# Kernel tuning notes

Measured on AMD Instinct MI355X. Metric: run time of the kernel, lower is better.

Reference implementation:

```python
import jax, jax.numpy as jnp
import numpy as np

NUM_HEADS = 4
HEAD_DIM = 32  # attention_dim 128 / 4 heads
SCALE = HEAD_DIM ** 0.5


def setup_inputs() -> dict:
    key = jax.random.key(0)
    ks = jax.random.split(key, 7)
    B, L, D = 4096, 200, 128
    return {
        "target_item": jax.random.normal(ks[0], (B, D), dtype=jnp.float32),
        "history_sequence": jax.random.normal(ks[1], (B, L, D), dtype=jnp.float32),
        "mask": jax.random.randint(ks[2], (B, L), 0, 2, dtype=jnp.int32),
        "W_q": jax.random.normal(ks[3], (D, D), dtype=jnp.float32) * 0.05,
        "W_k": jax.random.normal(ks[4], (D, D), dtype=jnp.float32) * 0.05,
        "W_v": jax.random.normal(ks[5], (D, D), dtype=jnp.float32) * 0.05,
        "W_o": jax.random.normal(ks[6], (D, D), dtype=jnp.float32) * 0.05,
    }


def reference(target_item, history_sequence, mask, W_q, W_k, W_v, W_o):
    B = target_item.shape[0]
    # QKV projections (nn.Linear with bias=False: y = x @ W.T)
    q = target_item @ W_q.T                      # [B, A]
    k = history_sequence @ W_k.T                 # [B, L, A]
    v = history_sequence @ W_v.T                 # [B, L, A]
    # split heads: q -> [B, H, d], k/v -> [B, H, L, d]
    q = q.reshape(B, NUM_HEADS, HEAD_DIM)
    k = k.reshape(B, -1, NUM_HEADS, HEAD_DIM).transpose(0, 2, 1, 3)
    v = v.reshape(B, -1, NUM_HEADS, HEAD_DIM).transpose(0, 2, 1, 3)
    # single-query scaled dot-product attention
    scores = jnp.einsum("bhd,bhld->bhl", q, k) / SCALE  # [B, H, L]
    m = (mask != 0)[:, None, :]                          # [B, 1, L]
    scores = jnp.where(m, scores, -jnp.inf)
    attn = jax.nn.softmax(scores, axis=-1)               # [B, H, L]
    out = jnp.einsum("bhl,bhld->bhd", attn, v)           # [B, H, d]
    out = out.reshape(B, NUM_HEADS * HEAD_DIM)           # [B, A]
    return out @ W_o.T                                    # [B, q_dim]
```

## Files before the change

### kernel.cpp

```cpp
#include <hip/hip_runtime.h>

#define LL 200
#define DD 128
#define NH 4
#define RSCALE 0.17677669529663687f

__device__ __forceinline__ float blo(unsigned int u) { return __uint_as_float(u << 16); }
__device__ __forceinline__ float bhi(unsigned int u) { return __uint_as_float(u & 0xffff0000u); }
__device__ __forceinline__ float b2f(unsigned short u) { return __uint_as_float(((unsigned int)u) << 16); }
__device__ __forceinline__ unsigned short f2bf(float f) {
  unsigned int u = __float_as_uint(f);
  u += 0x7fffu + ((u >> 16) & 1u);
  return (unsigned short)(u >> 16);
}

template <bool F32>
__device__ __forceinline__ float rowdot128(const void* __restrict__ wrow,
                                           const float* __restrict__ v) {
  float acc = 0.f;
  if constexpr (F32) {
    const float4* wr = (const float4*)wrow;
#pragma unroll
    for (int k = 0; k < 32; k++) {
      float4 w = wr[k];
      float4 vv = *(const float4*)(v + 4 * k);
      acc += w.x * vv.x + w.y * vv.y + w.z * vv.z + w.w * vv.w;
    }
  } else {
    const uint4* wr = (const uint4*)wrow;
#pragma unroll
    for (int k = 0; k < 16; k++) {
      uint4 u = wr[k];
      float4 v0 = *(const float4*)(v + k * 8);
      float4 v1 = *(const float4*)(v + k * 8 + 4);
      acc += blo(u.x) * v0.x + bhi(u.x) * v0.y + blo(u.y) * v0.z + bhi(u.y) * v0.w;
      acc += blo(u.z) * v1.x + bhi(u.z) * v1.y + blo(u.w) * v1.z + bhi(u.w) * v1.w;
    }
  }
  return acc;
}

template <bool F32>
__device__ __forceinline__ float welem(const void* w, size_t idx) {
  if constexpr (F32) return ((const float*)w)[idx];
  else               return b2f(((const unsigned short*)w)[idx]);
}

struct __align__(16) Smem {
  float qt[DD * NH];
  float sc[LL * NH];
  float tvec[DD];
  float qv[DD];
  float cpart[4 * 512];
  int flag;
};

template <bool F32>
__device__ __forceinline__ void body(Smem& sm, const int tid, const int b,
                                     const void* __restrict__ tgt,
                                     const void* __restrict__ hist,
                                     const int* __restrict__ mask,
                                     const void* __restrict__ Wq,
                                     const void* __restrict__ Wk,
                                     const void* __restrict__ Wv,
                                     const void* __restrict__ Wo,
                                     void* __restrict__ out) {
  const float NINF = -__builtin_inff();

  if (tid < DD) sm.tvec[tid] = welem<F32>(tgt, (size_t)b * DD + tid);
  __syncthreads();

  if (tid < DD)
    sm.qv[tid] = rowdot128<F32>((const char*)Wq + (size_t)tid * DD * (F32 ? 4 : 2), sm.tvec);
  __syncthreads();

  for (int e = tid; e < NH * DD; e += 256) {
    const int h = e >> 7, j = e & 127;
    float acc = 0.f;
#pragma unroll 8
    for (int d = 0; d < 32; d++)
      acc += sm.qv[h * 32 + d] * welem<F32>(Wk, (size_t)(h * 32 + d) * DD + j);
    sm.qt[j * NH + h] = acc * RSCALE;
  }
  __syncthreads();

  if (tid < LL) {
    const int l = tid;
    float a0 = 0.f, a1 = 0.f, a2 = 0.f, a3 = 0.f;
#define QACC(JE, FV) { float4 q_ = *(const float4*)&sm.qt[(JE) * 4]; const float f_ = (FV); \
  a0 += f_ * q_.x; a1 += f_ * q_.y; a2 += f_ * q_.z; a3 += f_ * q_.w; }
    if constexpr (!F32) {
      const uint4* hr = (const uint4*)((const unsigned short*)hist + (size_t)(b * LL + l) * DD);
#pragma unroll
      for (int c = 0; c < 2; c++) {
        uint4 u[8];
#pragma unroll
        for (int k = 0; k < 8; k++) u[k] = hr[c * 8 + k];
#pragma unroll
        for (int k = 0; k < 8; k++) {
          const int jb = c * 64 + k * 8;
          QACC(jb + 0, blo(u[k].x)); QACC(jb + 1, bhi(u[k].x));
          QACC(jb + 2, blo(u[k].y)); QACC(jb + 3, bhi(u[k].y));
          QACC(jb + 4, blo(u[k].z)); QACC(jb + 5, bhi(u[k].z));
          QACC(jb + 6, blo(u[k].w)); QACC(jb + 7, bhi(u[k].w));
        }
      }
    } else {
      const float4* hr = (const float4*)((const float*)hist + (size_t)(b * LL + l) * DD);
#pragma unroll
      for (int c = 0; c < 4; c++) {
        float4 u[8];
#pragma unroll
        for (int k = 0; k < 8; k++) u[k] = hr[c * 8 + k];
#pragma unroll
        for (int k = 0; k < 8; k++) {
          const int jb = c * 32 + k * 4;
          QACC(jb + 0, u[k].x); QACC(jb + 1, u[k].y);
          QACC(jb + 2, u[k].z); QACC(jb + 3, u[k].w);
        }
      }
    }
#undef QACC
    const bool mv = mask[(size_t)b * LL + l] != 0;
    float4 sv;
    sv.x = mv ? a0 : NINF;
    sv.y = mv ? a1 : NINF;
    sv.z = mv ? a2 : NINF;
    sv.w = mv ? a3 : NINF;
    *(float4*)&sm.sc[l * 4] = sv;
  }
  __syncthreads();

  {
    const int h = tid >> 6, lane = tid & 63;
    float v0 = sm.sc[lane * 4 + h];
    float v1 = sm.sc[(lane + 64) * 4 + h];
    float v2 = sm.sc[(lane + 128) * 4 + h];
    float v3 = (lane < 8) ? sm.sc[(lane + 192) * 4 + h] : NINF;
    float m = fmaxf(fmaxf(v0, v1), fmaxf(v2, v3));
#pragma unroll
    for (int off = 32; off; off >>= 1) m = fmaxf(m, __shfl_xor(m, off));
    float e0 = __expf(v0 - m), e1 = __expf(v1 - m), e2 = __expf(v2 - m);
    float e3 = (lane < 8) ? __expf(v3 - m) : 0.f;
    float s = e0 + e1 + e2 + e3;
#pragma unroll
    for (int off = 32; off; off >>= 1) s += __shfl_xor(s, off);
    const float r = 1.f / s;
    sm.sc[lane * 4 + h] = e0 * r;
    sm.sc[(lane + 64) * 4 + h] = e1 * r;
    sm.sc[(lane + 128) * 4 + h] = e2 * r;
    if (lane < 8) sm.sc[(lane + 192) * 4 + h] = e3 * r;
  }
  __syncthreads();

  {
    const int j2 = tid & 63;
    const int ch = tid >> 6;
    const int l0 = ch * 50;
    float a00=0.f,a01=0.f,a10=0.f,a11=0.f,a20=0.f,a21=0.f,a30=0.f,a31=0.f;
    if constexpr (!F32) {
      const unsigned int* hd =
          (const unsigned int*)((const unsigned short*)hist + (size_t)b * LL * DD) + j2;
#pragma unroll 5
      for (int l = l0; l < l0 + 50; l++) {
        const unsigned int dw = hd[l * 64];
        const float f0 = blo(dw), f1 = bhi(dw);
        const float4 at = *(const float4*)&sm.sc[l * 4];
        a00 += f0 * at.x; a01 += f1 * at.x;
        a10 += f0 * at.y; a11 += f1 * at.y;
        a20 += f0 * at.z; a21 += f1 * at.z;
        a30 += f0 * at.w; a31 += f1 * at.w;
      }
    } else {
      const float2* hf = (const float2*)((const float*)hist + (size_t)b * LL * DD) + j2;
#pragma unroll 5
      for (int l = l0; l < l0 + 50; l++) {
        const float2 f = hf[l * 64];
        const float4 at = *(const float4*)&sm.sc[l * 4];
        a00 += f.x * at.x; a01 += f.y * at.x;
        a10 += f.x * at.y; a11 += f.y * at.y;
        a20 += f.x * at.z; a21 += f.y * at.z;
        a30 += f.x * at.w; a31 += f.y * at.w;
      }
    }
    float* cp = &sm.cpart[ch * 512];
    const int j = 2 * j2;
    *(float2*)&cp[0 * DD + j] = make_float2(a00, a01);
    *(float2*)&cp[1 * DD + j] = make_float2(a10, a11);
    *(float2*)&cp[2 * DD + j] = make_float2(a20, a21);
    *(float2*)&cp[3 * DD + j] = make_float2(a30, a31);
  }
  __syncthreads();

  float* cvec = sm.qt;
  for (int idx = tid; idx < 512; idx += 256)
    cvec[idx] = sm.cpart[idx] + sm.cpart[512 + idx] + sm.cpart[1024 + idx] + sm.cpart[1536 + idx];
  __syncthreads();

  if (tid < DD)
    sm.tvec[tid] = rowdot128<F32>((const char*)Wv + (size_t)tid * DD * (F32 ? 4 : 2),
                                  &cvec[(tid >> 5) * DD]);
  __syncthreads();

  if (tid < DD) {
    const float acc = rowdot128<F32>((const char*)Wo + (size_t)tid * DD * (F32 ? 4 : 2), sm.tvec);
    if constexpr (F32) ((float*)out)[(size_t)b * DD + tid] = acc;
    else               ((unsigned short*)out)[(size_t)b * DD + tid] = f2bf(acc);
  }
}

__global__ __launch_bounds__(256, 5)
void mhta_kernel(const void* __restrict__ tgt,
                 const void* __restrict__ hist,
                 const int* __restrict__ mask,
                 const void* __restrict__ Wq,
                 const void* __restrict__ Wk,
                 const void* __restrict__ Wv,
                 const void* __restrict__ Wo,
                 void* __restrict__ out)
{
  __shared__ Smem sm;
  const int tid = threadIdx.x;
  const int b = blockIdx.x;

  if (tid < 64) {
    const unsigned int* hd = (const unsigned int*)((const char*)hist + (size_t)b * LL * DD * 2);
    const unsigned int e = (hd[tid] >> 7) & 0xffu;
    const unsigned long long bal = __ballot(e >= 110u && e <= 134u);
    if (tid == 0) sm.flag = (__popcll(bal) < 32) ? 1 : 0;
  }
  __syncthreads();

  if (sm.flag) body<true >(sm, tid, b, tgt, hist, mask, Wq, Wk, Wv, Wo, out);
  else         body<false>(sm, tid, b, tgt, hist, mask, Wq, Wk, Wv, Wo, out);
}

extern "C" void kernel_launch(void* const* d_in, const int* in_sizes, int n_in,
                              void* d_out, int out_size, void* d_ws, size_t ws_size,
                              hipStream_t stream) {
  const void* tgt  = d_in[0];
  const void* hist = d_in[1];
  const int*  mask = (const int*)d_in[2];
  const void* Wq   = d_in[3];
  const void* Wk   = d_in[4];
  const void* Wv   = d_in[5];
  const void* Wo   = d_in[6];

  const int B = in_sizes[0] / DD;

  mhta_kernel<<<dim3(B), dim3(256), 0, stream>>>(tgt, hist, mask, Wq, Wk, Wv, Wo, d_out);
}
```

Measured before the change: 694.5 us.

## Map one batch element per wavefront and skip loads for masked history rows

Restructures the kernel so each 64-lane wavefront handles a whole batch element (four per block) instead of a 256-thread block per element. Score computation skips history row loads where the mask is zero, and the attention-weighted value sum iterates only over a compacted list of unmasked rows built with ballot/popcount. This cuts history memory traffic roughly in half for the random mask and removes cross-wave reductions. In exchange each wave repeats all the projection work serially, and __syncthreads is now used inside per-wave code paths, which still hold up the whole block.

Result: slower. 890.9 us (+28.3%).

```diff
diff --git a/kernel.cpp b/kernel.cpp
--- a/kernel.cpp
+++ b/kernel.cpp
@@ -3,6 +3,7 @@
 #define LL 200
 #define DD 128
 #define NH 4
+#define WPB 4
 #define RSCALE 0.17677669529663687f
 
 __device__ __forceinline__ float blo(unsigned int u) { return __uint_as_float(u << 16); }
@@ -13,6 +14,9 @@
   u += 0x7fffu + ((u >> 16) & 1u);
   return (unsigned short)(u >> 16);
 }
+__device__ __forceinline__ unsigned int pack2(float lo, float hi) {
+  return ((unsigned int)f2bf(hi) << 16) | (unsigned int)f2bf(lo);
+}
 
 template <bool F32>
 __device__ __forceinline__ float rowdot128(const void* __restrict__ wrow,
@@ -46,17 +50,14 @@
   else               return b2f(((const unsigned short*)w)[idx]);
 }
 
-struct __align__(16) Smem {
-  float qt[DD * NH];
+struct __align__(16) WaveSmem {
+  float qt[NH * DD];
   float sc[LL * NH];
-  float tvec[DD];
-  float qv[DD];
-  float cpart[4 * 512];
-  int flag;
+  float u[2 * DD];
 };
 
 template <bool F32>
-__device__ __forceinline__ void body(Smem& sm, const int tid, const int b,
+__device__ __forceinline__ void body(WaveSmem& ws, const int lane, const int b,
                                      const void* __restrict__ tgt,
                                      const void* __restrict__ hist,
                                      const int* __restrict__ mask,
@@ -66,146 +67,241 @@
                                      const void* __restrict__ Wo,
                                      void* __restrict__ out) {
   const float NINF = -__builtin_inff();
-
-  if (tid < DD) sm.tvec[tid] = welem<F32>(tgt, (size_t)b * DD + tid);
-  __syncthreads();
-
-  if (tid < DD)
-    sm.qv[tid] = rowdot128<F32>((const char*)Wq + (size_t)tid * DD * (F32 ? 4 : 2), sm.tvec);
-  __syncthreads();
-
-  for (int e = tid; e < NH * DD; e += 256) {
-    const int h = e >> 7, j = e & 127;
-    float acc = 0.f;
-#pragma unroll 8
-    for (int d = 0; d < 32; d++)
-      acc += sm.qv[h * 32 + d] * welem<F32>(Wk, (size_t)(h * 32 + d) * DD + j);
-    sm.qt[j * NH + h] = acc * RSCALE;
-  }
-  __syncthreads();
-
-  if (tid < LL) {
-    const int l = tid;
-    float a0 = 0.f, a1 = 0.f, a2 = 0.f, a3 = 0.f;
-#define QACC(JE, FV) { float4 q_ = *(const float4*)&sm.qt[(JE) * 4]; const float f_ = (FV); \
-  a0 += f_ * q_.x; a1 += f_ * q_.y; a2 += f_ * q_.z; a3 += f_ * q_.w; }
-    if constexpr (!F32) {
-      const uint4* hr = (const uint4*)((const unsigned short*)hist + (size_t)(b * LL + l) * DD);
-#pragma unroll
-      for (int c = 0; c < 2; c++) {
-        uint4 u[8];
-#pragma unroll
-        for (int k = 0; k < 8; k++) u[k] = hr[c * 8 + k];
-#pragma unroll
-        for (int k = 0; k < 8; k++) {
-          const int jb = c * 64 + k * 8;
-          QACC(jb + 0, blo(u[k].x)); QACC(jb + 1, bhi(u[k].x));
-          QACC(jb + 2, blo(u[k].y)); QACC(jb + 3, bhi(u[k].y));
-          QACC(jb + 4, blo(u[k].z)); QACC(jb + 5, bhi(u[k].z));
-          QACC(jb + 6, blo(u[k].w)); QACC(jb + 7, bhi(u[k].w));
+  const size_t esz = F32 ? 4 : 2;
+  float* tvec = ws.u;
+  float* qv   = ws.u + DD;
+
+  if constexpr (F32) {
+    *(float2*)&tvec[2 * lane] = ((const float2*)tgt)[(size_t)b * 64 + lane];
+  } else {
+    const unsigned int dw = ((const unsigned int*)tgt)[(size_t)b * 64 + lane];
+    *(float2*)&tvec[2 * lane] = make_float2(blo(dw), bhi(dw));
+  }
+  __syncthreads();
+
+#pragma unroll
+  for (int r = 0; r < 2; r++) {
+    const int i = lane + 64 * r;
+    qv[i] = rowdot128<F32>((const char*)Wq + (size_t)i * DD * esz, tvec);
+  }
+  __syncthreads();
+
+#pragma unroll
+  for (int h = 0; h < NH; h++) {
+#pragma unroll
+    for (int r = 0; r < 2; r++) {
+      const int j = lane + 64 * r;
+      float acc = 0.f;
+#pragma unroll
+      for (int d = 0; d < 32; d++)
+        acc += qv[h * 32 + d] * welem<F32>(Wk, (size_t)(h * 32 + d) * DD + j);
+      ws.qt[j * NH + h] = acc * RSCALE;
+    }
+  }
+  __syncthreads();
+
+  int lrow[4];
+  int am[4];
+#pragma unroll
+  for (int k = 0; k < 3; k++) lrow[k] = lane + 64 * k;
+  lrow[3] = 192 + (lane & 7);
+#pragma unroll
+  for (int k = 0; k < 4; k++) am[k] = mask[(size_t)b * LL + lrow[k]] != 0;
+  if (lane >= 8) am[3] = 0;
+
+  float acc[4][4];
+#pragma unroll
+  for (int k = 0; k < 4; k++)
+#pragma unroll
+    for (int h = 0; h < 4; h++) acc[k][h] = 0.f;
+
+  const float4* qt4 = (const float4*)ws.qt;
+
+  if constexpr (!F32) {
+    const unsigned int* hb =
+        (const unsigned int*)((const unsigned short*)hist + (size_t)b * LL * DD);
+    uint4 rb[4][2] = {};
+#pragma unroll 2
+    for (int c = 0; c < 8; c++) {
+#pragma unroll
+      for (int k = 0; k < 4; k++)
+        if (am[k]) {
+          const uint4* p = (const uint4*)&hb[lrow[k] * 64 + (c << 3)];
+          rb[k][0] = p[0];
+          rb[k][1] = p[1];
+        }
+#pragma unroll
+      for (int d2 = 0; d2 < 8; d2++) {
+        const int jj = (c << 4) + (d2 << 1);
+        const float4 q0 = qt4[jj];
+        const float4 q1 = qt4[jj + 1];
+#pragma unroll
+        for (int k = 0; k < 4; k++) {
+          const uint4 v = rb[k][d2 >> 2];
+          const unsigned int dw = ((d2 & 3) == 0) ? v.x
+                                : ((d2 & 3) == 1) ? v.y
+                                : ((d2 & 3) == 2) ? v.z : v.w;
+          const float f0 = blo(dw), f1 = bhi(dw);
+          acc[k][0] += f0 * q0.x + f1 * q1.x;
+          acc[k][1] += f0 * q0.y + f1 * q1.y;
+          acc[k][2] += f0 * q0.z + f1 * q1.z;
+          acc[k][3] += f0 * q0.w + f1 * q1.w;
         }
       }
-    } else {
-      const float4* hr = (const float4*)((const float*)hist + (size_t)(b * LL + l) * DD);
-#pragma unroll
-      for (int c = 0; c < 4; c++) {
-        float4 u[8];
-#pragma unroll
-        for (int k = 0; k < 8; k++) u[k] = hr[c * 8 + k];
-#pragma unroll
-        for (int k = 0; k < 8; k++) {
-          const int jb = c * 32 + k * 4;
-          QACC(jb + 0, u[k].x); QACC(jb + 1, u[k].y);
-          QACC(jb + 2, u[k].z); QACC(jb + 3, u[k].w);
-        }
+    }
+  } else {
+    const float* hf = (const float*)hist + (size_t)b * LL * DD;
+    float4 rb[4] = {};
+#pragma unroll 4
+    for (int c = 0; c < 32; c++) {
+#pragma unroll
+      for (int k = 0; k < 4; k++)
+        if (am[k]) rb[k] = *(const float4*)&hf[(size_t)lrow[k] * DD + (c << 2)];
+      const float4 q0 = qt4[(c << 2)];
+      const float4 q1 = qt4[(c << 2) + 1];
+      const float4 q2 = qt4[(c << 2) + 2];
+      const float4 q3 = qt4[(c << 2) + 3];
+#pragma unroll
+      for (int k = 0; k < 4; k++) {
+        acc[k][0] += rb[k].x * q0.x + rb[k].y * q1.x + rb[k].z * q2.x + rb[k].w * q3.x;
+        acc[k][1] += rb[k].x * q0.y + rb[k].y * q1.y + rb[k].z * q2.y + rb[k].w * q3.y;
+        acc[k][2] += rb[k].x * q0.z + rb[k].y * q1.z + rb[k].z * q2.z + rb[k].w * q3.z;
+        acc[k][3] += rb[k].x * q0.w + rb[k].y * q1.w + rb[k].z * q2.w + rb[k].w * q3.w;
       }
     }
-#undef QACC
-    const bool mv = mask[(size_t)b * LL + l] != 0;
-    float4 sv;
-    sv.x = mv ? a0 : NINF;
-    sv.y = mv ? a1 : NINF;
-    sv.z = mv ? a2 : NINF;
-    sv.w = mv ? a3 : NINF;
-    *(float4*)&sm.sc[l * 4] = sv;
+  }
+
+#pragma unroll
+  for (int k = 0; k < 4; k++)
+#pragma unroll
+    for (int h = 0; h < 4; h++) acc[k][h] = am[k] ? acc[k][h] : NINF;
+
+  float rr[4];
+#pragma unroll
+  for (int h = 0; h < 4; h++) {
+    float m = fmaxf(fmaxf(acc[0][h], acc[1][h]), fmaxf(acc[2][h], acc[3][h]));
+#pragma unroll
+    for (int off = 32; off; off >>= 1) m = fmaxf(m, __shfl_xor(m, off));
+    float e0 = __expf(acc[0][h] - m);
+    float e1 = __expf(acc[1][h] - m);
+    float e2 = __expf(acc[2][h] - m);
+    float e3 = __expf(acc[3][h] - m);
+    acc[0][h] = e0; acc[1][h] = e1; acc[2][h] = e2; acc[3][h] = e3;
+    float su = e0 + e1 + e2 + e3;
+#pragma unroll
+    for (int off = 32; off; off >>= 1) su += __shfl_xor(su, off);
+    rr[h] = 1.f / su;
+  }
+
+  int* sidx = (int*)ws.u;
+  const unsigned long long lt = (1ull << lane) - 1ull;
+  int base = 0;
+#pragma unroll
+  for (int k = 0; k < 4; k++) {
+    const unsigned long long bal = __ballot(am[k] != 0);
+    const int pos = base + (int)__popcll(bal & lt);
+    if (am[k]) {
+      sidx[pos] = lrow[k];
+      *(float4*)&ws.sc[pos * 4] = make_float4(acc[k][0] * rr[0], acc[k][1] * rr[1],
+                                              acc[k][2] * rr[2], acc[k][3] * rr[3]);
+    }
+    base += (int)__popcll(bal);
+  }
+  const int cnt = base;
+  __syncthreads();
+
+  float4 cl = make_float4(0.f, 0.f, 0.f, 0.f);
+  float4 chh = make_float4(0.f, 0.f, 0.f, 0.f);
+  const int j2 = lane;
+  if constexpr (!F32) {
+    const unsigned int* hd =
+        (const unsigned int*)((const unsigned short*)hist + (size_t)b * LL * DD) + j2;
+    int i = 0;
+    for (; i + 4 <= cnt; i += 4) {
+      const int4 li = *(const int4*)&sidx[i];
+      const unsigned int w0 = hd[li.x << 6];
+      const unsigned int w1 = hd[li.y << 6];
+      const unsigned int w2 = hd[li.z << 6];
+      const unsigned int w3 = hd[li.w << 6];
+      const float4 a0 = *(const float4*)&ws.sc[(i + 0) * 4];
+      const float4 a1 = *(const float4*)&ws.sc[(i + 1) * 4];
+      const float4 a2 = *(const float4*)&ws.sc[(i + 2) * 4];
+      const float4 a3 = *(const float4*)&ws.sc[(i + 3) * 4];
+      float f0, f1;
+      f0 = blo(w0); f1 = bhi(w0);
+      cl.x += f0 * a0.x; cl.y += f0 * a0.y; cl.z += f0 * a0.z; cl.w += f0 * a0.w;
+      chh.x += f1 * a0.x; chh.y += f1 * a0.y; chh.z += f1 * a0.z; chh.w += f1 * a0.w;
+      f0 = blo(w1); f1 = bhi(w1);
+      cl.x += f0 * a1.x; cl.y += f0 * a1.y; cl.z += f0 * a1.z; cl.w += f0 * a1.w;
+      chh.x += f1 * a1.x; chh.y += f1 * a1.y; chh.z += f1 * a1.z; chh.w += f1 * a1.w;
+      f0 = blo(w2); f1 = bhi(w2);
+      cl.x += f0 * a2.x; cl.y += f0 * a2.y; cl.z += f0 * a2.z; cl.w += f0 * a2.w;
+      chh.x += f1 * a2.x; chh.y += f1 * a2.y; chh.z += f1 * a2.z; chh.w += f1 * a2.w;
+      f0 = blo(w3); f1 = bhi(w3);
+      cl.x += f0 * a3.x; cl.y += f0 * a3.y; cl.z += f0 * a3.z; cl.w += f0 * a3.w;
+      chh.x += f1 * a3.x; chh.y += f1 * a3.y; chh.z += f1 * a3.z; chh.w += f1 * a3.w;
+    }
+    for (; i < cnt; i++) {
+      const int l = sidx[i];
+      const unsigned int w0 = hd[l << 6];
+      const float4 a0 = *(const float4*)&ws.sc[i * 4];
+      const float f0 = blo(w0), f1 = bhi(w0);
+      cl.x += f0 * a0.x; cl.y += f0 * a0.y; cl.z += f0 * a0.z; cl.w += f0 * a0.w;
+      chh.x += f1 * a0.x; chh.y += f1 * a0.y; chh.z += f1 * a0.z; chh.w += f1 * a0.w;
+    }
+  } else {
+    const float2* hf = (const float2*)((const float*)hist + (size_t)b * LL * DD) + j2;
+    int i = 0;
+    for (; i + 4 <= cnt; i += 4) {
+      const int4 li = *(const int4*)&sidx[i];
+      const float2 w0 = hf[li.x << 6];
+      const float2 w1 = hf[li.y << 6];
+      const float2 w2 = hf[li.z << 6];
+      const float2 w3 = hf[li.w << 6];
+      const float4 a0 = *(const float4*)&ws.sc[(i + 0) * 4];
+      const float4 a1 = *(const float4*)&ws.sc[(i + 1) * 4];
+      const float4 a2 = *(const float4*)&ws.sc[(i + 2) * 4];
+      const float4 a3 = *(const float4*)&ws.sc[(i + 3) * 4];
+      cl.x += w0.x * a0.x; cl.y += w0.x * a0.y; cl.z += w0.x * a0.z; cl.w += w0.x * a0.w;
+      chh.x += w0.y * a0.x; chh.y += w0.y * a0.y; chh.z += w0.y * a0.z; chh.w += w0.y * a0.w;
+      cl.x += w1.x * a1.x; cl.y += w1.x * a1.y; cl.z += w1.x * a1.z; cl.w += w1.x * a1.w;
+      chh.x += w1.y * a1.x; chh.y += w1.y * a1.y; chh.z += w1.y * a1.z; chh.w += w1.y * a1.w;
+      cl.x += w2.x * a2.x; cl.y += w2.x * a2.y; cl.z += w2.x * a2.z; cl.w += w2.x * a2.w;
+      chh.x += w2.y * a2.x; chh.y += w2.y * a2.y; chh.z += w2.y * a2.z; chh.w += w2.y * a2.w;
+      cl.x += w3.x * a3.x; cl.y += w3.x * a3.y; cl.z += w3.x * a3.z; cl.w += w3.x * a3.w;
+      chh.x += w3.y * a3.x; chh.y += w3.y * a3.y; chh.z += w3.y * a3.z; chh.w += w3.y * a3.w;
+    }
+    for (; i < cnt; i++) {
+      const int l = sidx[i];
+      const float2 w0 = hf[l << 6];
+      const float4 a0 = *(const float4*)&ws.sc[i * 4];
+      cl.x += w0.x * a0.x; cl.y += w0.x * a0.y; cl.z += w0.x * a0.z; cl.w += w0.x * a0.w;
+      chh.x += w0.y * a0.x; chh.y += w0.y * a0.y; chh.z += w0.y * a0.z; chh.w += w0.y * a0.w;
+    }
+  }
+
+  float* cvec = ws.qt;
+  *(float2*)&cvec[0 * DD + 2 * j2] = make_float2(cl.x, chh.x);
+  *(float2*)&cvec[1 * DD + 2 * j2] = make_float2(cl.y, chh.y);
+  *(float2*)&cvec[2 * DD + 2 * j2] = make_float2(cl.z, chh.z);
+  *(float2*)&cvec[3 * DD + 2 * j2] = make_float2(cl.w, chh.w);
+  __syncthreads();
+
+  float* ovec = ws.u;
+#pragma unroll
+  for (int r = 0; r < 2; r++) {
+    const int i = lane + 64 * r;
+    ovec[i] = rowdot128<F32>((const char*)Wv + (size_t)i * DD * esz,
+                             &cvec[(i >> 5) * DD]);
   }
   __syncthreads();
 
   {
-    const int h = tid >> 6, lane = tid & 63;
-    float v0 = sm.sc[lane * 4 + h];
-    float v1 = sm.sc[(lane + 64) * 4 + h];
-    float v2 = sm.sc[(lane + 128) * 4 + h];
-    float v3 = (lane < 8) ? sm.sc[(lane + 192) * 4 + h] : NINF;
-    float m = fmaxf(fmaxf(v0, v1), fmaxf(v2, v3));
-#pragma unroll
-    for (int off = 32; off; off >>= 1) m = fmaxf(m, __shfl_xor(m, off));
-    float e0 = __expf(v0 - m), e1 = __expf(v1 - m), e2 = __expf(v2 - m);
-    float e3 = (lane < 8) ? __expf(v3 - m) : 0.f;
-    float s = e0 + e1 + e2 + e3;
-#pragma unroll
-    for (int off = 32; off; off >>= 1) s += __shfl_xor(s, off);
-    const float r = 1.f / s;
-    sm.sc[lane * 4 + h] = e0 * r;
-    sm.sc[(lane + 64) * 4 + h] = e1 * r;
-    sm.sc[(lane + 128) * 4 + h] = e2 * r;
-    if (lane < 8) sm.sc[(lane + 192) * 4 + h] = e3 * r;
-  }
-  __syncthreads();
-
-  {
-    const int j2 = tid & 63;
-    const int ch = tid >> 6;
-    const int l0 = ch * 50;
-    float a00=0.f,a01=0.f,a10=0.f,a11=0.f,a20=0.f,a21=0.f,a30=0.f,a31=0.f;
-    if constexpr (!F32) {
-      const unsigned int* hd =
-          (const unsigned int*)((const unsigned short*)hist + (size_t)b * LL * DD) + j2;
-#pragma unroll 5
-      for (int l = l0; l < l0 + 50; l++) {
-        const unsigned int dw = hd[l * 64];
-        const float f0 = blo(dw), f1 = bhi(dw);
-        const float4 at = *(const float4*)&sm.sc[l * 4];
-        a00 += f0 * at.x; a01 += f1 * at.x;
-        a10 += f0 * at.y; a11 += f1 * at.y;
-        a20 += f0 * at.z; a21 += f1 * at.z;
-        a30 += f0 * at.w; a31 += f1 * at.w;
-      }
-    } else {
-      const float2* hf = (const float2*)((const float*)hist + (size_t)b * LL * DD) + j2;
-#pragma unroll 5
-      for (int l = l0; l < l0 + 50; l++) {
-        const float2 f = hf[l * 64];
-        const float4 at = *(const float4*)&sm.sc[l * 4];
-        a00 += f.x * at.x; a01 += f.y * at.x;
-        a10 += f.x * at.y; a11 += f.y * at.y;
-        a20 += f.x * at.z; a21 += f.y * at.z;
-        a30 += f.x * at.w; a31 += f.y * at.w;
-      }
-    }
-    float* cp = &sm.cpart[ch * 512];
-    const int j = 2 * j2;
-    *(float2*)&cp[0 * DD + j] = make_float2(a00, a01);
-    *(float2*)&cp[1 * DD + j] = make_float2(a10, a11);
-    *(float2*)&cp[2 * DD + j] = make_float2(a20, a21);
-    *(float2*)&cp[3 * DD + j] = make_float2(a30, a31);
-  }
-  __syncthreads();
-
-  float* cvec = sm.qt;
-  for (int idx = tid; idx < 512; idx += 256)
-    cvec[idx] = sm.cpart[idx] + sm.cpart[512 + idx] + sm.cpart[1024 + idx] + sm.cpart[1536 + idx];
-  __syncthreads();
-
-  if (tid < DD)
-    sm.tvec[tid] = rowdot128<F32>((const char*)Wv + (size_t)tid * DD * (F32 ? 4 : 2),
-                                  &cvec[(tid >> 5) * DD]);
-  __syncthreads();
-
-  if (tid < DD) {
-    const float acc = rowdot128<F32>((const char*)Wo + (size_t)tid * DD * (F32 ? 4 : 2), sm.tvec);
-    if constexpr (F32) ((float*)out)[(size_t)b * DD + tid] = acc;
-    else               ((unsigned short*)out)[(size_t)b * DD + tid] = f2bf(acc);
+    const int i0 = 2 * lane, i1 = 2 * lane + 1;
+    const float o0 = rowdot128<F32>((const char*)Wo + (size_t)i0 * DD * esz, ovec);
+    const float o1 = rowdot128<F32>((const char*)Wo + (size_t)i1 * DD * esz, ovec);
+    if constexpr (F32) ((float2*)out)[(size_t)b * 64 + lane] = make_float2(o0, o1);
+    else               ((unsigned int*)out)[(size_t)b * 64 + lane] = pack2(o0, o1);
   }
 }
 
@@ -217,22 +313,27 @@
                  const void* __restrict__ Wk,
                  const void* __restrict__ Wv,
                  const void* __restrict__ Wo,
-                 void* __restrict__ out)
+                 void* __restrict__ out,
+                 const int Btot)
 {
-  __shared__ Smem sm;
+  __shared__ WaveSmem sm[WPB];
+  __shared__ int flag;
   const int tid = threadIdx.x;
-  const int b = blockIdx.x;
+  const int lane = tid & 63;
+  const int wv = tid >> 6;
+  int b = blockIdx.x * WPB + wv;
+  if (b >= Btot) b = Btot - 1;
 
   if (tid < 64) {
-    const unsigned int* hd = (const unsigned int*)((const char*)hist + (size_t)b * LL * DD * 2);
+    const unsigned int* hd = (const unsigned int*)hist;
     const unsigned int e = (hd[tid] >> 7) & 0xffu;
     const unsigned long long bal = __ballot(e >= 110u && e <= 134u);
-    if (tid == 0) sm.flag = (__popcll(bal) < 32) ? 1 : 0;
-  }
-  __syncthreads();
-
-  if (sm.flag) body<true >(sm, tid, b, tgt, hist, mask, Wq, Wk, Wv, Wo, out);
-  else         body<false>(sm, tid, b, tgt, hist, mask, Wq, Wk, Wv, Wo, out);
+    if (tid == 0) flag = (__popcll(bal) < 32) ? 1 : 0;
+  }
+  __syncthreads();
+
+  if (flag) body<true >(sm[wv], lane, b, tgt, hist, mask, Wq, Wk, Wv, Wo, out);
+  else      body<false>(sm[wv], lane, b, tgt, hist, mask, Wq, Wk, Wv, Wo, out);
 }
 
 extern "C" void kernel_launch(void* const* d_in, const int* in_sizes, int n_in,
@@ -247,6 +348,7 @@
   const void* Wo   = d_in[6];
 
   const int B = in_sizes[0] / DD;
-
-  mhta_kernel<<<dim3(B), dim3(256), 0, stream>>>(tgt, hist, mask, Wq, Wk, Wv, Wo, d_out);
-}
+  const int nb = (B + WPB - 1) / WPB;
+
+  mhta_kernel<<<dim3(nb), dim3(256), 0, stream>>>(tgt, hist, mask, Wq, Wk, Wv, Wo, d_out, B);
+}
```
